# Kernel optimization log

Hardware: AMD Instinct MI355X
Metric: run time of the kernel (lower is better)

## Reference

```python
import jax, jax.numpy as jnp
import numpy as np

N = 100_000   # nodes
E = 1_600_000 # edges
F = 128       # featurenum
H = 32        # hidden size (hard-coded in module)
G = 256       # graphs in batch


def setup_inputs() -> dict:
    key = jax.random.key(0)
    ks = jax.random.split(key, 10)
    x = jax.random.normal(ks[0], (N, F), jnp.float32)
    edge_index = jax.random.randint(ks[1], (2, E), 0, N)
    edge_attr = jax.random.randint(ks[2], (E, 1), 0, 4)
    batch = jnp.sort(jax.random.randint(ks[3], (N,), 0, G))
    def w(k, shape, fan):
        return jax.random.normal(k, shape, jnp.float32) / np.float32(np.sqrt(fan))
    W1 = w(ks[4], (F, H), F); b1 = jnp.zeros((H,), jnp.float32)
    W2 = w(ks[5], (H, H), H); b2 = jnp.zeros((H,), jnp.float32)
    Wl = w(ks[6], (H, 4 * H), H); bl = jnp.zeros((4 * H,), jnp.float32)
    Wm1 = w(ks[7], (H, H), H); bm1 = jnp.zeros((H,), jnp.float32)
    Wm2 = w(ks[8], (H, 1), H); bm2 = jnp.zeros((1,), jnp.float32)
    return dict(x=x, edge_index=edge_index, edge_attr=edge_attr, batch=batch,
                W1=W1, b1=b1, W2=W2, b2=b2, Wl=Wl, bl=bl,
                Wm1=Wm1, bm1=bm1, Wm2=Wm2, bm2=bm2)


def gcn_conv(x, src, tgt, W, b, n):
    # PyG GCNConv: add self-loops, symmetric normalization D^-1/2 (A+I) D^-1/2
    xw = x @ W                                            # [n, out]
    ones = jnp.ones(tgt.shape[0], x.dtype)
    deg = jax.ops.segment_sum(ones, tgt, num_segments=n) + 1.0  # in-degree + self-loop
    dinv = jax.lax.rsqrt(deg)
    msg = (dinv[src] * dinv[tgt])[:, None] * xw[src]      # [E, out]
    out = jax.ops.segment_sum(msg, tgt, num_segments=n)
    out = out + xw * (1.0 / deg)[:, None]                 # self-loop term (norm = 1/deg)
    return out + b


def reference(x, edge_index, edge_attr, batch, W1, b1, W2, b2, Wl, bl, Wm1, bm1, Wm2, bm2):
    n = x.shape[0]
    src, tgt = edge_index[0], edge_index[1]
    h = jax.nn.relu(gcn_conv(x, src, tgt, W1, b1, n))
    h = jax.nn.relu(gcn_conv(h, src, tgt, W2, b2, n))
    # MPNNl: linear -> (n, 4, H), gather slot per edge, scatter-mean to targets
    hl = (h @ Wl + bl).reshape(n, 4, H)
    rs = hl[src, edge_attr[:, 0]]                         # [E, H]
    cnt = jax.ops.segment_sum(jnp.ones(tgt.shape[0], h.dtype), tgt, num_segments=n)
    agg = jax.ops.segment_sum(rs, tgt, num_segments=n) / jnp.maximum(cnt, 1.0)[:, None]
    # global mean pool over graphs
    gcnt = jax.ops.segment_sum(jnp.ones(n, h.dtype), batch, num_segments=G)
    g = jax.ops.segment_sum(agg, batch, num_segments=G) / jnp.maximum(gcnt, 1.0)[:, None]
    # dropout in eval mode = identity; MLP + sigmoid
    out = jax.nn.relu(g @ Wm1 + bm1) @ Wm2 + bm2
    return jax.nn.sigmoid(out)                            # [G, 1]
```

## Files before the change

### kernel.cpp

```cpp
#include <hip/hip_runtime.h>
#include <hip/hip_bf16.h>
#include <stdint.h>

#define CDIV(a, b) (((a) + (b) - 1) / (b))

constexpr int BSH = 9;
#define TILE_A 2048

__global__ __launch_bounds__(256) void coarse_hist_k(const int* __restrict__ tgt,
                                                     int* __restrict__ bcnt, int E, int nb) {
    __shared__ int h[512];
    int t = threadIdx.x;
    for (int i = t; i < nb; i += 256) h[i] = 0;
    __syncthreads();
    for (int e = blockIdx.x * 256 + t; e < E; e += gridDim.x * 256)
        atomicAdd(&h[tgt[e] >> BSH], 1);
    __syncthreads();
    for (int i = t; i < nb; i += 256)
        if (h[i]) atomicAdd(&bcnt[i], h[i]);
}

__global__ __launch_bounds__(256) void bucket_scan_k(const int* __restrict__ bcnt,
                                                     int* __restrict__ bbase,
                                                     int* __restrict__ bcur, int nb, int E) {
    __shared__ int sp[256];
    int t = threadIdx.x;
    int c0 = (2 * t < nb) ? bcnt[2 * t] : 0;
    int c1 = (2 * t + 1 < nb) ? bcnt[2 * t + 1] : 0;
    int s2 = c0 + c1;
    sp[t] = s2;
    __syncthreads();
    for (int off = 1; off < 256; off <<= 1) {
        int x = (t >= off) ? sp[t - off] : 0;
        __syncthreads();
        sp[t] += x;
        __syncthreads();
    }
    int excl = sp[t] - s2;
    if (2 * t < nb) { bbase[2 * t] = excl; bcur[2 * t] = excl; }
    if (2 * t + 1 < nb) { bbase[2 * t + 1] = excl + c0; bcur[2 * t + 1] = excl + c0; }
    if (t == 0) bbase[nb] = E;
}

__global__ __launch_bounds__(256) void binA_k(const int* __restrict__ ei,
                                              const int* __restrict__ ea,
                                              int* __restrict__ bcur,
                                              unsigned long long* __restrict__ tmp, int E) {
    __shared__ unsigned long long stage[TILE_A];
    __shared__ int h_cnt[512], h_excl[512], h_cur[512], h_run[512], sp[256];
    int t = threadIdx.x;
    int base = blockIdx.x * TILE_A;
    int nt = min(TILE_A, E - base);
    for (int i = t; i < 512; i += 256) { h_cnt[i] = 0; h_cur[i] = 0; }
    __syncthreads();
    unsigned long long pk[8];
    int bk[8];
#pragma unroll
    for (int k = 0; k < 8; ++k) {
        int e = base + t + k * 256;
        bk[k] = -1;
        if (e < E) {
            int s = ei[e], tg = ei[E + e];
            unsigned a = (unsigned)ea[e];
            pk[k] = ((unsigned long long)(unsigned)tg << 20) |
                    ((unsigned long long)a << 18) | (unsigned long long)(unsigned)s;
            bk[k] = tg >> BSH;
            atomicAdd(&h_cnt[bk[k]], 1);
        }
    }
    __syncthreads();
    int c0 = h_cnt[2 * t], c1 = h_cnt[2 * t + 1];
    int s2 = c0 + c1;
    sp[t] = s2;
    __syncthreads();
    for (int off = 1; off < 256; off <<= 1) {
        int x = (t >= off) ? sp[t - off] : 0;
        __syncthreads();
        sp[t] += x;
        __syncthreads();
    }
    int excl = sp[t] - s2;
    h_excl[2 * t] = excl;
    h_excl[2 * t + 1] = excl + c0;
    __syncthreads();
    for (int i = t; i < 512; i += 256)
        if (h_cnt[i]) h_run[i] = atomicAdd(&bcur[i], h_cnt[i]);
#pragma unroll
    for (int k = 0; k < 8; ++k) {
        if (bk[k] >= 0) {
            int r = atomicAdd(&h_cur[bk[k]], 1);
            stage[h_excl[bk[k]] + r] = pk[k];
        }
    }
    __syncthreads();
    for (int i = t; i < nt; i += 256) {
        unsigned long long v = stage[i];
        int b = (int)(v >> 20) >> BSH;
        tmp[h_run[b] + (i - h_excl[b])] = v;
    }
}

__global__ __launch_bounds__(256) void binB_k(const unsigned long long* __restrict__ tmp,
                                              const int* __restrict__ bbase,
                                              unsigned* __restrict__ adj,
                                              int* __restrict__ rowptr4,
                                              float* __restrict__ dinv, int N, int E) {
    __shared__ int ncnt4[2048], nbase4[2048], ncur4[2048], sp[256];
    int t = threadIdx.x, b = blockIdx.x;
    int e0 = bbase[b], e1 = bbase[b + 1];
    int node0 = b << BSH;
    int nn = min(512, N - node0);
    for (int i = t; i < 2048; i += 256) { ncnt4[i] = 0; ncur4[i] = 0; }
    __syncthreads();
    for (int e = e0 + t; e < e1; e += 256) {
        unsigned long long v = tmp[e];
        int li = (int)(v >> 20) - node0;
        int q = (int)(v >> 18) & 3;
        atomicAdd(&ncnt4[li * 4 + q], 1);
    }
    __syncthreads();
    int loc[8];
    int s = 0;
#pragma unroll
    for (int k = 0; k < 8; ++k) { loc[k] = ncnt4[t * 8 + k]; s += loc[k]; }
    sp[t] = s;
    __syncthreads();
    for (int off = 1; off < 256; off <<= 1) {
        int x = (t >= off) ? sp[t - off] : 0;
        __syncthreads();
        sp[t] += x;
        __syncthreads();
    }
    int run = sp[t] - s;
#pragma unroll
    for (int k = 0; k < 8; ++k) { nbase4[t * 8 + k] = run; run += loc[k]; }
    __syncthreads();
    for (int i = t; i < nn; i += 256) {
        int node = node0 + i;
        *(int4*)&rowptr4[node * 4] = make_int4(e0 + nbase4[i * 4], e0 + nbase4[i * 4 + 1],
                                               e0 + nbase4[i * 4 + 2], e0 + nbase4[i * 4 + 3]);
        int c = ncnt4[i * 4] + ncnt4[i * 4 + 1] + ncnt4[i * 4 + 2] + ncnt4[i * 4 + 3];
        dinv[node] = rsqrtf((float)c + 1.0f);
    }
    if (b == 0 && t == 0) rowptr4[N * 4] = E;
    for (int e = e0 + t; e < e1; e += 256) {
        unsigned long long v = tmp[e];
        int li = (int)(v >> 20) - node0;
        int q = (int)(v >> 18) & 3;
        int r = atomicAdd(&ncur4[li * 4 + q], 1);
        adj[e0 + nbase4[li * 4 + q] + r] = (unsigned)(v & 0x3FFFFull);
    }
}

__device__ __forceinline__ int lb_sorted(const int* __restrict__ b, int n, int g) {
    int lo = 0, hi = n;
    while (lo < hi) {
        int m = (lo + hi) >> 1;
        if (b[m] < g) lo = m + 1; else hi = m;
    }
    return lo;
}

__global__ __launch_bounds__(256) void gbounds_k(const int* __restrict__ batch,
                                                 int* __restrict__ gcnt, int n, int Gn) {
    int g = blockIdx.x * 256 + threadIdx.x;
    if (g < Gn) {
        int a = lb_sorted(batch, n, g);
        int b2 = lb_sorted(batch, n, g + 1);
        gcnt[g] = b2 - a;
    }
}

template <int K, int COUT, int R>
__global__ __launch_bounds__(256) void gemm_rk(const float* __restrict__ X,
                                               const float* __restrict__ W,
                                               const float* __restrict__ bias,
                                               float* __restrict__ Y, int nrows) {
    constexpr int NCG = COUT / 8;
    constexpr int RG = 256 / NCG;
    constexpr int ROWS = RG * R;
    constexpr int WS = K + 5;
    __shared__ float wt[COUT][WS];
    int t = threadIdx.x;
    for (int i = t; i < K * COUT; i += 256) {
        int k = i / COUT, j = i % COUT;
        wt[j][k] = W[i];
    }
    __syncthreads();
    int cg = t % NCG, g = t / NCG;
    int j0 = cg * 8;
    long rowbase = (long)blockIdx.x * ROWS + (long)g * R;
    float acc[R][8];
#pragma unroll
    for (int r = 0; r < R; ++r)
#pragma unroll
        for (int j = 0; j < 8; ++j) acc[r][j] = 0.0f;

    long rr[R];
#pragma unroll
    for (int r = 0; r < R; ++r) {
        long q = rowbase + r;
        rr[r] = (q < nrows) ? q : (long)(nrows - 1);
    }
    for (int k0 = 0; k0 < K; k0 += 4) {
        float4 xv[R];
#pragma unroll
        for (int r = 0; r < R; ++r) xv[r] = *(const float4*)(X + rr[r] * K + k0);
        float4 wv[8];
#pragma unroll
        for (int j = 0; j < 8; ++j) wv[j] = *(const float4*)&wt[j0 + j][k0];
#pragma unroll
        for (int r = 0; r < R; ++r)
#pragma unroll
            for (int j = 0; j < 8; ++j) {
                acc[r][j] += xv[r].x * wv[j].x;
                acc[r][j] += xv[r].y * wv[j].y;
                acc[r][j] += xv[r].z * wv[j].z;
                acc[r][j] += xv[r].w * wv[j].w;
            }
    }
#pragma unroll
    for (int r = 0; r < R; ++r) {
        long row = rowbase + r;
        if (row < nrows) {
            float o[8];
#pragma unroll
            for (int j = 0; j < 8; ++j) {
                float v = acc[r][j];
                if (bias) v += bias[j0 + j];
                o[j] = v;
            }
            float4 o0 = make_float4(o[0], o[1], o[2], o[3]);
            float4 o1 = make_float4(o[4], o[5], o[6], o[7]);
            *(float4*)&Y[row * COUT + j0] = o0;
            *(float4*)&Y[row * COUT + j0 + 4] = o1;
        }
    }
}


__device__ __forceinline__ void store_feat(float* p, float v) { *p = v; }
__device__ __forceinline__ void store_feat(ushort* p, float v) {
    __hip_bfloat16 b = __float2bfloat16(v);
    *p = *reinterpret_cast<ushort*>(&b);
}

template <typename OutT>
__global__ __launch_bounds__(256) void agg_conv_k(const float* __restrict__ xw,
                                                  const unsigned* __restrict__ adj,
                                                  const int* __restrict__ rowptr4,
                                                  const float* __restrict__ dinv,
                                                  const float* __restrict__ bias,
                                                  OutT* __restrict__ out, int n) {
    int t = threadIdx.x;
    int node = blockIdx.x * 8 + (t >> 5);
    int f = t & 31;
    if (node >= n) return;
    int e0 = rowptr4[node * 4];
    int e1 = rowptr4[node * 4 + 4];
    float a0 = 0.0f, a1 = 0.0f, a2 = 0.0f, a3 = 0.0f;
    int e = e0;
    for (; e + 3 < e1; e += 4) {
        int s0 = adj[e], s1 = adj[e + 1], s2 = adj[e + 2], s3 = adj[e + 3];
        a0 += dinv[s0] * xw[s0 * 32 + f];
        a1 += dinv[s1] * xw[s1 * 32 + f];
        a2 += dinv[s2] * xw[s2 * 32 + f];
        a3 += dinv[s3] * xw[s3 * 32 + f];
    }
    for (; e < e1; ++e) {
        int s = adj[e];
        a0 += dinv[s] * xw[s * 32 + f];
    }
    float degv = (float)(e1 - e0) + 1.0f;
    float v = dinv[node] * ((a0 + a1) + (a2 + a3)) + xw[node * 32 + f] * (1.0f / degv) + bias[f];
    store_feat(&out[node * 32 + f], fmaxf(v, 0.0f));
}

__device__ __forceinline__ float bf2f(ushort u) {
    return __uint_as_float(((unsigned)u) << 16);
}

__global__ __launch_bounds__(256) void agg_rs_fused_k(const ushort* __restrict__ h2,
                                                      const unsigned* __restrict__ adj,
                                                      const int* __restrict__ rowptr4,
                                                      const float* __restrict__ Wl,
                                                      const float* __restrict__ bl,
                                                      float* __restrict__ out, int n) {
    __shared__ float wls[32][128];
    __shared__ float bls[128];
    __shared__ float accs[8][128];
    int t = threadIdx.x;
    for (int i = t; i < 4096; i += 256) wls[i >> 7][i & 127] = Wl[i];
    if (t < 128) bls[t] = bl[t];
    __syncthreads();

    int nl = t >> 5;
    int f = t & 31;
    int node = blockIdx.x * 8 + nl;
    if (node >= n) return;
    int4 rp = *(const int4*)&rowptr4[node * 4];
    int e4 = rowptr4[node * 4 + 4];
    float a0 = 0.f, a1 = 0.f, a2 = 0.f, a3 = 0.f;
    int e = rp.x;
    for (; e + 3 < e4; e += 4) {
        int s0 = adj[e], s1 = adj[e + 1], s2 = adj[e + 2], s3 = adj[e + 3];
        float v0 = bf2f(h2[s0 * 32 + f]);
        float v1 = bf2f(h2[s1 * 32 + f]);
        float v2 = bf2f(h2[s2 * 32 + f]);
        float v3 = bf2f(h2[s3 * 32 + f]);
        int q0 = (e >= rp.y) + (e >= rp.z) + (e >= rp.w);
        int q1 = (e + 1 >= rp.y) + (e + 1 >= rp.z) + (e + 1 >= rp.w);
        int q2 = (e + 2 >= rp.y) + (e + 2 >= rp.z) + (e + 2 >= rp.w);
        int q3 = (e + 3 >= rp.y) + (e + 3 >= rp.z) + (e + 3 >= rp.w);
        a0 += (q0 == 0) ? v0 : 0.f; a1 += (q0 == 1) ? v0 : 0.f;
        a2 += (q0 == 2) ? v0 : 0.f; a3 += (q0 == 3) ? v0 : 0.f;
        a0 += (q1 == 0) ? v1 : 0.f; a1 += (q1 == 1) ? v1 : 0.f;
        a2 += (q1 == 2) ? v1 : 0.f; a3 += (q1 == 3) ? v1 : 0.f;
        a0 += (q2 == 0) ? v2 : 0.f; a1 += (q2 == 1) ? v2 : 0.f;
        a2 += (q2 == 2) ? v2 : 0.f; a3 += (q2 == 3) ? v2 : 0.f;
        a0 += (q3 == 0) ? v3 : 0.f; a1 += (q3 == 1) ? v3 : 0.f;
        a2 += (q3 == 2) ? v3 : 0.f; a3 += (q3 == 3) ? v3 : 0.f;
    }
    for (; e < e4; ++e) {
        int s = adj[e];
        float v = bf2f(h2[s * 32 + f]);
        int q = (e >= rp.y) + (e >= rp.z) + (e >= rp.w);
        a0 += (q == 0) ? v : 0.f; a1 += (q == 1) ? v : 0.f;
        a2 += (q == 2) ? v : 0.f; a3 += (q == 3) ? v : 0.f;
    }

    accs[nl][f] = a0;
    accs[nl][32 + f] = a1;
    accs[nl][64 + f] = a2;
    accs[nl][96 + f] = a3;
    float m0 = (float)(rp.y - rp.x), m1 = (float)(rp.z - rp.y);
    float m2 = (float)(rp.w - rp.z), m3 = (float)(e4 - rp.w);
    float o = m0 * bls[f] + m1 * bls[32 + f] + m2 * bls[64 + f] + m3 * bls[96 + f];
#pragma unroll 8
    for (int j = 0; j < 32; ++j) {
        o += accs[nl][j] * wls[j][f] + accs[nl][32 + j] * wls[j][32 + f] +
             accs[nl][64 + j] * wls[j][64 + f] + accs[nl][96 + j] * wls[j][96 + f];
    }
    float c = (float)(e4 - rp.x);
    out[node * 32 + f] = o / fmaxf(c, 1.0f);
}


__global__ __launch_bounds__(256) void graph_sum_k(const float* __restrict__ agg,
                                                   const int* __restrict__ batch,
                                                   float* __restrict__ gsum, int n) {
    const int CHUNK = 128;
    int t = threadIdx.x;
    int f = t & 31;
    int j = t >> 5;
    long base = (long)blockIdx.x * (8 * CHUNK) + (long)j * CHUNK;
    if (base >= n) return;
    int end = (int)((n - base < CHUNK) ? (n - base) : CHUNK);
    int cur = batch[base];
    float acc = 0.0f;
    for (int i = 0; i < end; ++i) {
        int b = batch[base + i];
        if (b != cur) {
            atomicAdd(&gsum[cur * 32 + f], acc);
            acc = 0.0f;
            cur = b;
        }
        acc += agg[(base + i) * 32 + f];
    }
    atomicAdd(&gsum[cur * 32 + f], acc);
}


__global__ __launch_bounds__(256) void mlp_k(const float* __restrict__ gsum,
                                             const int* __restrict__ gcnt,
                                             const float* __restrict__ Wm1,
                                             const float* __restrict__ bm1,
                                             const float* __restrict__ Wm2,
                                             const float* __restrict__ bm2,
                                             float* __restrict__ out, int Gn) {
    __shared__ float w1[1024];
    __shared__ float w2[32];
    __shared__ float b1s[32];
    int t = threadIdx.x;
    for (int i = t; i < 1024; i += 256) w1[i] = Wm1[i];
    if (t < 32) {
        w2[t] = Wm2[t];
        b1s[t] = bm1[t];
    }
    __syncthreads();
    if (t < Gn) {
        float inv = 1.0f / fmaxf((float)gcnt[t], 1.0f);
        float gm[32];
#pragma unroll
        for (int k = 0; k < 32; ++k) gm[k] = gsum[t * 32 + k] * inv;
        float o = bm2[0];
        for (int j = 0; j < 32; ++j) {
            float h = b1s[j];
#pragma unroll
            for (int k = 0; k < 32; ++k) h += gm[k] * w1[k * 32 + j];
            o += fmaxf(h, 0.0f) * w2[j];
        }
        out[t] = 1.0f / (1.0f + expf(-o));
    }
}


extern "C" void kernel_launch(void* const* d_in, const int* in_sizes, int n_in,
                              void* d_out, int out_size, void* d_ws, size_t ws_size,
                              hipStream_t stream) {
    const float* x = (const float*)d_in[0];
    const int* ei = (const int*)d_in[1];
    const int* ea = (const int*)d_in[2];
    const int* batch = (const int*)d_in[3];
    const float* W1 = (const float*)d_in[4];
    const float* b1 = (const float*)d_in[5];
    const float* W2 = (const float*)d_in[6];
    const float* b2 = (const float*)d_in[7];
    const float* Wl = (const float*)d_in[8];
    const float* bl = (const float*)d_in[9];
    const float* Wm1 = (const float*)d_in[10];
    const float* bm1 = (const float*)d_in[11];
    const float* Wm2 = (const float*)d_in[12];
    const float* bm2 = (const float*)d_in[13];

    const int N = in_sizes[3];
    const int E = in_sizes[2];
    const int Gn = out_size;
    const int NBUCKET = CDIV(N, 512);

    char* ws = (char*)d_ws;
    size_t off = 0;
    auto alloc = [&](size_t bytes) -> void* {
        void* p = ws + off;
        off = (off + bytes + 255) & ~(size_t)255;
        return p;
    };
    int* rowptr4 = (int*)alloc((size_t)(4 * N + 4) * 4);
    float* dinv = (float*)alloc((size_t)N * 4);
    int* bcnt = (int*)alloc(512 * 4);
    int* bbase = (int*)alloc(513 * 4);
    int* bcur = (int*)alloc(512 * 4);
    unsigned* adj = (unsigned*)alloc((size_t)E * 4);
    float* gsum = (float*)alloc((size_t)Gn * 32 * 4);
    int* gcnt = (int*)alloc((size_t)Gn * 4);
    float* bufA = (float*)alloc((size_t)N * 32 * 4);
    float* bufB = (float*)alloc((size_t)N * 32 * 4);
    ushort* h2bf = (ushort*)alloc((size_t)N * 32 * 2);
    unsigned long long* tmp = (unsigned long long*)alloc((size_t)E * 8);

    if (off > ws_size || NBUCKET > 512) return;

    hipMemsetAsync(bcnt, 0, 512 * 4, stream);
    hipMemsetAsync(gsum, 0, (size_t)Gn * 32 * 4, stream);

    coarse_hist_k<<<400, 256, 0, stream>>>(ei + E, bcnt, E, NBUCKET);
    bucket_scan_k<<<1, 256, 0, stream>>>(bcnt, bbase, bcur, NBUCKET, E);
    binA_k<<<CDIV(E, TILE_A), 256, 0, stream>>>(ei, ea, bcur, tmp, E);
    binB_k<<<NBUCKET, 256, 0, stream>>>(tmp, bbase, adj, rowptr4, dinv, N, E);
    gbounds_k<<<CDIV(Gn, 256), 256, 0, stream>>>(batch, gcnt, N, Gn);

    gemm_rk<128, 32, 1><<<CDIV(N, 64), 256, 0, stream>>>(x, W1, nullptr, bufA, N);
    agg_conv_k<float><<<CDIV(N, 8), 256, 0, stream>>>(bufA, adj, rowptr4, dinv, b1, bufB, N);
    gemm_rk<32, 32, 1><<<CDIV(N, 64), 256, 0, stream>>>(bufB, W2, nullptr, bufA, N);
    agg_conv_k<ushort><<<CDIV(N, 8), 256, 0, stream>>>(bufA, adj, rowptr4, dinv, b2, h2bf, N);
    agg_rs_fused_k<<<CDIV(N, 8), 256, 0, stream>>>(h2bf, adj, rowptr4, Wl, bl, bufA, N);
    graph_sum_k<<<CDIV(N, 1024), 256, 0, stream>>>(bufA, batch, gsum, N);
    mlp_k<<<1, 256, 0, stream>>>(gsum, gcnt, Wm1, bm1, Wm2, bm2, (float*)d_out, Gn);
}
```

Before: 353.4 us.

## Pre-scale GEMM output by dinv in bf16 and pack edge slot into adj

The GCN GEMMs now multiply each output row by the source node's dinv and store it as bf16. This removes the per-edge dinv gather and halves the bytes gathered per edge in both aggregation kernels; the self-loop term is rescaled to undo the folded factor. The adjacency entries also keep the 2-bit edge-attr slot in their high bits, so the MPNN aggregation reads the slot directly instead of comparing against row pointers. The cost is bf16 rounding of the intermediate features before aggregation.

```diff
diff --git a/kernel.cpp b/kernel.cpp
--- a/kernel.cpp
+++ b/kernel.cpp
@@ -148,7 +148,7 @@
         int li = (int)(v >> 20) - node0;
         int q = (int)(v >> 18) & 3;
         int r = atomicAdd(&ncur4[li * 4 + q], 1);
-        adj[e0 + nbase4[li * 4 + q] + r] = (unsigned)(v & 0x3FFFFull);
+        adj[e0 + nbase4[li * 4 + q] + r] = (unsigned)(v & 0xFFFFFull);
     }
 }
 
@@ -171,11 +171,20 @@
     }
 }
 
-template <int K, int COUT, int R>
+__device__ __forceinline__ ushort f2bf(float v) {
+    __hip_bfloat16 b = __float2bfloat16(v);
+    return *reinterpret_cast<ushort*>(&b);
+}
+__device__ __forceinline__ float bf2f(ushort u) {
+    return __uint_as_float(((unsigned)u) << 16);
+}
+
+template <int K, int COUT, int R, typename OutT>
 __global__ __launch_bounds__(256) void gemm_rk(const float* __restrict__ X,
                                                const float* __restrict__ W,
                                                const float* __restrict__ bias,
-                                               float* __restrict__ Y, int nrows) {
+                                               const float* __restrict__ dinv,
+                                               OutT* __restrict__ Y, int nrows) {
     constexpr int NCG = COUT / 8;
     constexpr int RG = 256 / NCG;
     constexpr int ROWS = RG * R;
@@ -223,30 +232,37 @@
     for (int r = 0; r < R; ++r) {
         long row = rowbase + r;
         if (row < nrows) {
+            float dv = dinv ? dinv[row] : 1.0f;
             float o[8];
 #pragma unroll
             for (int j = 0; j < 8; ++j) {
                 float v = acc[r][j];
                 if (bias) v += bias[j0 + j];
-                o[j] = v;
+                o[j] = v * dv;
             }
-            float4 o0 = make_float4(o[0], o[1], o[2], o[3]);
-            float4 o1 = make_float4(o[4], o[5], o[6], o[7]);
-            *(float4*)&Y[row * COUT + j0] = o0;
-            *(float4*)&Y[row * COUT + j0 + 4] = o1;
+            if constexpr (sizeof(OutT) == 4) {
+                float4 o0 = make_float4(o[0], o[1], o[2], o[3]);
+                float4 o1 = make_float4(o[4], o[5], o[6], o[7]);
+                *(float4*)&Y[row * COUT + j0] = o0;
+                *(float4*)&Y[row * COUT + j0 + 4] = o1;
+            } else {
+                uint4 u;
+                u.x = (unsigned)f2bf(o[0]) | ((unsigned)f2bf(o[1]) << 16);
+                u.y = (unsigned)f2bf(o[2]) | ((unsigned)f2bf(o[3]) << 16);
+                u.z = (unsigned)f2bf(o[4]) | ((unsigned)f2bf(o[5]) << 16);
+                u.w = (unsigned)f2bf(o[6]) | ((unsigned)f2bf(o[7]) << 16);
+                *(uint4*)&Y[row * COUT + j0] = u;
+            }
         }
     }
 }
 
 
 __device__ __forceinline__ void store_feat(float* p, float v) { *p = v; }
-__device__ __forceinline__ void store_feat(ushort* p, float v) {
-    __hip_bfloat16 b = __float2bfloat16(v);
-    *p = *reinterpret_cast<ushort*>(&b);
-}
+__device__ __forceinline__ void store_feat(ushort* p, float v) { *p = f2bf(v); }
 
 template <typename OutT>
-__global__ __launch_bounds__(256) void agg_conv_k(const float* __restrict__ xw,
+__global__ __launch_bounds__(256) void agg_conv_k(const ushort* __restrict__ xwd,
                                                   const unsigned* __restrict__ adj,
                                                   const int* __restrict__ rowptr4,
                                                   const float* __restrict__ dinv,
@@ -261,23 +277,22 @@
     float a0 = 0.0f, a1 = 0.0f, a2 = 0.0f, a3 = 0.0f;
     int e = e0;
     for (; e + 3 < e1; e += 4) {
-        int s0 = adj[e], s1 = adj[e + 1], s2 = adj[e + 2], s3 = adj[e + 3];
-        a0 += dinv[s0] * xw[s0 * 32 + f];
-        a1 += dinv[s1] * xw[s1 * 32 + f];
-        a2 += dinv[s2] * xw[s2 * 32 + f];
-        a3 += dinv[s3] * xw[s3 * 32 + f];
+        int s0 = adj[e] & 0x3FFFF, s1 = adj[e + 1] & 0x3FFFF;
+        int s2 = adj[e + 2] & 0x3FFFF, s3 = adj[e + 3] & 0x3FFFF;
+        a0 += bf2f(xwd[s0 * 32 + f]);
+        a1 += bf2f(xwd[s1 * 32 + f]);
+        a2 += bf2f(xwd[s2 * 32 + f]);
+        a3 += bf2f(xwd[s3 * 32 + f]);
     }
     for (; e < e1; ++e) {
-        int s = adj[e];
-        a0 += dinv[s] * xw[s * 32 + f];
-    }
+        int s = adj[e] & 0x3FFFF;
+        a0 += bf2f(xwd[s * 32 + f]);
+    }
+    float dvn = dinv[node];
     float degv = (float)(e1 - e0) + 1.0f;
-    float v = dinv[node] * ((a0 + a1) + (a2 + a3)) + xw[node * 32 + f] * (1.0f / degv) + bias[f];
+    float sself = 1.0f / (dvn * degv);
+    float v = dvn * ((a0 + a1) + (a2 + a3)) + bf2f(xwd[node * 32 + f]) * sself + bias[f];
     store_feat(&out[node * 32 + f], fmaxf(v, 0.0f));
-}
-
-__device__ __forceinline__ float bf2f(ushort u) {
-    return __uint_as_float(((unsigned)u) << 16);
 }
 
 __global__ __launch_bounds__(256) void agg_rs_fused_k(const ushort* __restrict__ h2,
@@ -303,15 +318,13 @@
     float a0 = 0.f, a1 = 0.f, a2 = 0.f, a3 = 0.f;
     int e = rp.x;
     for (; e + 3 < e4; e += 4) {
-        int s0 = adj[e], s1 = adj[e + 1], s2 = adj[e + 2], s3 = adj[e + 3];
+        unsigned u0 = adj[e], u1 = adj[e + 1], u2 = adj[e + 2], u3 = adj[e + 3];
+        int s0 = u0 & 0x3FFFF, s1 = u1 & 0x3FFFF, s2 = u2 & 0x3FFFF, s3 = u3 & 0x3FFFF;
+        int q0 = u0 >> 18, q1 = u1 >> 18, q2 = u2 >> 18, q3 = u3 >> 18;
         float v0 = bf2f(h2[s0 * 32 + f]);
         float v1 = bf2f(h2[s1 * 32 + f]);
         float v2 = bf2f(h2[s2 * 32 + f]);
         float v3 = bf2f(h2[s3 * 32 + f]);
-        int q0 = (e >= rp.y) + (e >= rp.z) + (e >= rp.w);
-        int q1 = (e + 1 >= rp.y) + (e + 1 >= rp.z) + (e + 1 >= rp.w);
-        int q2 = (e + 2 >= rp.y) + (e + 2 >= rp.z) + (e + 2 >= rp.w);
-        int q3 = (e + 3 >= rp.y) + (e + 3 >= rp.z) + (e + 3 >= rp.w);
         a0 += (q0 == 0) ? v0 : 0.f; a1 += (q0 == 1) ? v0 : 0.f;
         a2 += (q0 == 2) ? v0 : 0.f; a3 += (q0 == 3) ? v0 : 0.f;
         a0 += (q1 == 0) ? v1 : 0.f; a1 += (q1 == 1) ? v1 : 0.f;
@@ -322,9 +335,10 @@
         a2 += (q3 == 2) ? v3 : 0.f; a3 += (q3 == 3) ? v3 : 0.f;
     }
     for (; e < e4; ++e) {
-        int s = adj[e];
+        unsigned u = adj[e];
+        int s = u & 0x3FFFF;
+        int q = u >> 18;
         float v = bf2f(h2[s * 32 + f]);
-        int q = (e >= rp.y) + (e >= rp.z) + (e >= rp.w);
         a0 += (q == 0) ? v : 0.f; a1 += (q == 1) ? v : 0.f;
         a2 += (q == 2) ? v : 0.f; a3 += (q == 3) ? v : 0.f;
     }
@@ -445,6 +459,7 @@
     int* gcnt = (int*)alloc((size_t)Gn * 4);
     float* bufA = (float*)alloc((size_t)N * 32 * 4);
     float* bufB = (float*)alloc((size_t)N * 32 * 4);
+    ushort* xw_bf = (ushort*)alloc((size_t)N * 32 * 2);
     ushort* h2bf = (ushort*)alloc((size_t)N * 32 * 2);
     unsigned long long* tmp = (unsigned long long*)alloc((size_t)E * 8);
 
@@ -459,10 +474,10 @@
     binB_k<<<NBUCKET, 256, 0, stream>>>(tmp, bbase, adj, rowptr4, dinv, N, E);
     gbounds_k<<<CDIV(Gn, 256), 256, 0, stream>>>(batch, gcnt, N, Gn);
 
-    gemm_rk<128, 32, 1><<<CDIV(N, 64), 256, 0, stream>>>(x, W1, nullptr, bufA, N);
-    agg_conv_k<float><<<CDIV(N, 8), 256, 0, stream>>>(bufA, adj, rowptr4, dinv, b1, bufB, N);
-    gemm_rk<32, 32, 1><<<CDIV(N, 64), 256, 0, stream>>>(bufB, W2, nullptr, bufA, N);
-    agg_conv_k<ushort><<<CDIV(N, 8), 256, 0, stream>>>(bufA, adj, rowptr4, dinv, b2, h2bf, N);
+    gemm_rk<128, 32, 1, ushort><<<CDIV(N, 64), 256, 0, stream>>>(x, W1, nullptr, dinv, xw_bf, N);
+    agg_conv_k<float><<<CDIV(N, 8), 256, 0, stream>>>(xw_bf, adj, rowptr4, dinv, b1, bufB, N);
+    gemm_rk<32, 32, 1, ushort><<<CDIV(N, 64), 256, 0, stream>>>(bufB, W2, nullptr, dinv, xw_bf, N);
+    agg_conv_k<ushort><<<CDIV(N, 8), 256, 0, stream>>>(xw_bf, adj, rowptr4, dinv, b2, h2bf, N);
     agg_rs_fused_k<<<CDIV(N, 8), 256, 0, stream>>>(h2bf, adj, rowptr4, Wl, bl, bufA, N);
     graph_sum_k<<<CDIV(N, 1024), 256, 0, stream>>>(bufA, batch, gsum, N);
     mlp_k<<<1, 256, 0, stream>>>(gsum, gcnt, Wm1, bm1, Wm2, bm2, (float*)d_out, Gn);
```

New measurement: 347.1 us. About the same (-1.8%).
